# Kernel optimization log

Measured on AMD Instinct MI355X. Metric: run time of the kernel, lower is better.

## Reference

```python
import jax, jax.numpy as jnp
import numpy as np

DN = ('NCDHW', 'OIDHW', 'NCDHW')  # conv dimension numbers for 3D conv in torch layout
EPS = 1e-14


def setup_inputs() -> dict:
    key = jax.random.key(0)
    k1, k2 = jax.random.split(key)
    # xs: [B, C, D, H, W]
    xs = jax.random.normal(k1, (16, 128, 24, 24, 24), dtype=jnp.float32)
    # feature_vectors (prototypes): [num_features, C, w_1, h_1, L_1]
    feature_vectors = jax.random.normal(k2, (128, 128, 3, 3, 3), dtype=jnp.float32)
    return {"xs": xs, "feature_vectors": feature_vectors}


def reference(xs, feature_vectors):
    F_, C, kd, kh, kw = feature_vectors.shape
    # ||x_patch||^2: the original convolves xs**2 with all-ones weights of shape
    # [F, C, kd, kh, kw], producing F identical channels. We compute a single
    # sum-pool channel (same math) and let broadcasting supply the F channels.
    ones = jnp.ones((1, C, kd, kh, kw), dtype=xs.dtype)
    xs_squared_l2 = jax.lax.conv_general_dilated(
        xs * xs, ones, window_strides=(1, 1, 1), padding='VALID',
        dimension_numbers=DN)  # [B, 1, D', H', W']
    # ||p||^2 per prototype: [F, 1, 1, 1]
    ps_squared_l2 = jnp.sum(feature_vectors * feature_vectors,
                            axis=(1, 2, 3, 4)).reshape(-1, 1, 1, 1)
    # <x_patch, p>: the real weighted conv. [B, F, D', H', W']
    xs_conv = jax.lax.conv_general_dilated(
        xs, feature_vectors, window_strides=(1, 1, 1), padding='VALID',
        dimension_numbers=DN)
    distance = xs_squared_l2 + ps_squared_l2 - 2.0 * xs_conv
    return jnp.sqrt(jnp.abs(distance) + EPS)
```

## Files before the change

kernel.cpp:

```cpp
#include <hip/hip_runtime.h>
#include <hip/hip_bf16.h>

typedef __attribute__((ext_vector_type(8))) __bf16 bf16x8;
typedef __attribute__((ext_vector_type(2))) __bf16 bf16x2;
typedef __attribute__((ext_vector_type(4))) float f32x4;

#define B_   16
#define C_   128
#define DIM  24
#define F_   128
#define OD   22
#define OS   (OD*OD*OD)
#define SPB  (DIM*DIM*DIM)
#define K_   3456
#define M_   (B_*OS)
#define OUTN (B_*F_*OS)

__device__ __forceinline__ void async16(const void* g, void* l) {
  __builtin_amdgcn_global_load_lds(
      (const __attribute__((address_space(1))) unsigned int*)g,
      (__attribute__((address_space(3))) unsigned int*)l, 16, 0, 0);
}

__global__ __launch_bounds__(256) void prep_x(const float* __restrict__ xs,
                                              __bf16* __restrict__ xt,
                                              float* __restrict__ s1) {
  __shared__ float tile[C_ * 97];
  __shared__ float red[192];
  const int blk = blockIdx.x;
  const int yg = blk % 6;
  const int t2 = blk / 6;
  const int z = t2 % DIM;
  const int b = t2 / DIM;
  const int t = threadIdx.x;
  const float* src = xs + (size_t)b * C_ * SPB + z * (DIM * DIM) + yg * 96;
  for (int it = 0; it < 12; ++it) {
    int idx = it * 256 + t;
    int c = idx / 24, f4 = idx - c * 24;
    const float4 v = *(const float4*)(src + (size_t)c * SPB + f4 * 4);
    float* d = &tile[c * 97 + f4 * 4];
    d[0] = v.x; d[1] = v.y; d[2] = v.z; d[3] = v.w;
  }
  __syncthreads();
  size_t obase = ((size_t)b * SPB + z * (DIM * DIM) + yg * 96) * C_;
  for (int it = 0; it < 24; ++it) {
    int idx = it * 256 + t;
    int c2 = idx & 63, x = idx >> 6;
    bf16x2 v;
    v[0] = (__bf16)tile[(2 * c2) * 97 + x];
    v[1] = (__bf16)tile[(2 * c2 + 1) * 97 + x];
    *(bf16x2*)&xt[obase + (size_t)x * C_ + 2 * c2] = v;
  }
  if (t < 192) {
    int g = t / 96, p = t - g * 96;
    float s = 0.f;
    for (int c = g; c < C_; c += 2) {
      float v = tile[c * 97 + p];
      s += v * v;
    }
    red[g * 96 + p] = s;
  }
  __syncthreads();
  if (t < 96)
    s1[((size_t)b * SPB + z * (DIM * DIM) + yg * 96) + t] = red[t] + red[96 + t];
}

__global__ void prep_w(const float* __restrict__ fv, __bf16* __restrict__ Wt,
                       float* __restrict__ psq) {
  __shared__ float tile[K_];
  const int f = blockIdx.x;
  const float* src = fv + (size_t)f * K_;
  float part = 0.f;
  for (int idx = threadIdx.x; idx < K_; idx += 256) {
    float v = src[idx];
    tile[idx] = v;
    part += v * v;
  }
  __syncthreads();
  for (int idx = threadIdx.x; idx < K_; idx += 256) {
    int c = idx & 127, off = idx >> 7;
    Wt[(size_t)f * K_ + idx] = (__bf16)tile[c * 27 + off];
  }
  for (int o = 32; o > 0; o >>= 1) part += __shfl_down(part, o, 64);
  __shared__ float red[4];
  int w = threadIdx.x >> 6, l = threadIdx.x & 63;
  if (l == 0) red[w] = part;
  __syncthreads();
  if (threadIdx.x == 0) psq[f] = red[0] + red[1] + red[2] + red[3];
}

__global__ void pool_sq(const float* __restrict__ s1, float* __restrict__ xsq) {
  int i = blockIdx.x * 256 + threadIdx.x;
  if (i >= M_) return;
  int ow = i % OD;
  int t = i / OD;
  int oh = t % OD; t /= OD;
  int od = t % OD;
  int b = t / OD;
  const float* p = s1 + ((b * DIM + od) * DIM + oh) * DIM + ow;
  float s = 0.f;
#pragma unroll
  for (int dz = 0; dz < 3; ++dz)
#pragma unroll
    for (int dy = 0; dy < 3; ++dy)
#pragma unroll
      for (int dx = 0; dx < 3; ++dx)
        s += p[dz * 576 + dy * 24 + dx];
  xsq[i] = s;
}

__global__ __launch_bounds__(256, 2) void l2gemm(
    const __bf16* __restrict__ xt, const __bf16* __restrict__ Wt,
    const float* __restrict__ xsq, const float* __restrict__ psq,
    float* __restrict__ out) {
  __shared__ __align__(16) __bf16 Wl[128 * 64];
  __shared__ __align__(16) __bf16 Pl[256 * 64];
  const int t = threadIdx.x;
  const int l = t & 63, w = t >> 6;
  const int quad = l >> 4, lan = l & 15;
  const int e = t & 7, r0 = t >> 3;
  const int esw = (e ^ (r0 & 7)) * 8;

  const int nwg = gridDim.x;
  const int orig = blockIdx.x;
  const int xcd = orig & 7, lo = orig >> 3;
  const int q = nwg >> 3, r = nwg & 7;
  const int mt = (xcd < r ? xcd * (q + 1) : r * (q + 1) + (xcd - r) * q) + lo;

  int sb[8];
#pragma unroll
  for (int p = 0; p < 8; ++p) {
    int m = mt * 256 + r0 + 32 * p;
    if (m >= M_) m = M_ - 1;
    int b = m / OS;
    int s = m - b * OS;
    int od = s / (OD * OD);
    int s2 = s - od * (OD * OD);
    int oh = s2 / OD;
    int ow = s2 - oh * OD;
    sb[p] = b * SPB + od * 576 + oh * 24 + ow;
  }

  f32x4 acc[4][8];
#pragma unroll
  for (int i = 0; i < 4; ++i)
#pragma unroll
    for (int n = 0; n < 8; ++n) acc[i][n] = (f32x4){0.f, 0.f, 0.f, 0.f};

  const int wm = (w & 1) * 64;
  const int wn = (w >> 1) * 128;

#pragma unroll 1
  for (int kt = 0; kt < 54; ++kt) {
    {
      int off = kt >> 1;
      int dz = off / 9;
      int rem = off - dz * 9;
      int dy = rem / 3;
      int dx = rem - dy * 3;
      int doff = dz * 576 + dy * 24 + dx;
      int c0 = (kt & 1) << 6;
#pragma unroll
      for (int p = 0; p < 4; ++p) {
        const __bf16* gw = Wt + (size_t)(r0 + 32 * p) * K_ + kt * 64 + esw;
        async16(gw, &Wl[(size_t)(8 * w + 32 * p) * 64]);
      }
#pragma unroll
      for (int p = 0; p < 8; ++p) {
        const __bf16* gp = xt + (((size_t)(sb[p] + doff)) << 7) + c0 + esw;
        async16(gp, &Pl[(size_t)(8 * w + 32 * p) * 64]);
      }
    }
    __syncthreads();
#pragma unroll
    for (int kk = 0; kk < 2; ++kk) {
      const int swz = ((kk * 4 + quad) ^ (lan & 7)) * 8;
      bf16x8 a[4], bb[8];
#pragma unroll
      for (int i = 0; i < 4; ++i)
        a[i] = *(const bf16x8*)&Wl[(wm + i * 16 + lan) * 64 + swz];
#pragma unroll
      for (int n = 0; n < 8; ++n)
        bb[n] = *(const bf16x8*)&Pl[(wn + n * 16 + lan) * 64 + swz];
      __builtin_amdgcn_s_setprio(1);
#pragma unroll
      for (int i = 0; i < 4; ++i)
#pragma unroll
        for (int n = 0; n < 8; ++n)
          acc[i][n] = __builtin_amdgcn_mfma_f32_16x16x32_bf16(a[i], bb[n],
                                                              acc[i][n], 0, 0, 0);
      __builtin_amdgcn_s_setprio(0);
    }
    __syncthreads();
  }

  int mb[8], mok[8];
  float xv[8];
#pragma unroll
  for (int n = 0; n < 8; ++n) {
    int m = mt * 256 + wn + n * 16 + lan;
    mok[n] = (m < M_);
    if (m >= M_) m = M_ - 1;
    int b = m / OS;
    int s = m - b * OS;
    mb[n] = b * (F_ * OS) + s;
    xv[n] = xsq[m];
  }
#pragma unroll
  for (int i = 0; i < 4; ++i) {
#pragma unroll
    for (int r2 = 0; r2 < 4; ++r2) {
      int f = wm + i * 16 + quad * 4 + r2;
      float pq = psq[f];
#pragma unroll
      for (int n = 0; n < 8; ++n) {
        if (mok[n]) {
          float d = xv[n] + pq - 2.0f * acc[i][n][r2];
          out[mb[n] + f * OS] = sqrtf(fabsf(d) + 1e-14f);
        }
      }
    }
  }
}

__global__ void l2conv_direct(const float* __restrict__ xs,
                              const float* __restrict__ fv,
                              float* __restrict__ out) {
  int i = blockIdx.x * 256 + threadIdx.x;
  if (i >= OUTN) return;
  int s = i % OS;
  int t2 = i / OS;
  int f = t2 & 127;
  int b = t2 >> 7;
  int od = s / (OD * OD);
  int s2 = s - od * (OD * OD);
  int oh = s2 / OD;
  int ow = s2 - oh * OD;
  const float* xp = xs + (size_t)b * C_ * SPB + od * 576 + oh * 24 + ow;
  const float* wp = fv + (size_t)f * K_;
  float dot = 0.f, xq = 0.f, pq = 0.f;
  for (int c = 0; c < C_; ++c) {
    const float* xpc = xp + (size_t)c * SPB;
    const float* wpc = wp + c * 27;
#pragma unroll
    for (int o = 0; o < 27; ++o) {
      int dz = o / 9;
      int ry = o - dz * 9;
      int dy = ry / 3;
      int dx = ry - dy * 3;
      float xv = xpc[dz * 576 + dy * 24 + dx];
      float wv = wpc[o];
      dot += xv * wv;
      xq += xv * xv;
      pq += wv * wv;
    }
  }
  out[i] = sqrtf(fabsf(xq + pq - 2.f * dot) + 1e-14f);
}

extern "C" void kernel_launch(void* const* d_in, const int* in_sizes, int n_in,
                              void* d_out, int out_size, void* d_ws,
                              size_t ws_size, hipStream_t stream) {
  const float* xs = (const float*)d_in[0];
  const float* fv = (const float*)d_in[1];
  float* out = (float*)d_out;

  const size_t xt_b  = (size_t)B_ * SPB * C_ * 2;
  const size_t wt_b  = (size_t)F_ * K_ * 2;
  const size_t s1_b  = (size_t)B_ * SPB * 4;
  const size_t xsq_b = (size_t)M_ * 4;
  const size_t psq_b = 512;
  if (ws_size < xt_b + wt_b + s1_b + xsq_b + psq_b) {
    l2conv_direct<<<(OUTN + 255) / 256, 256, 0, stream>>>(xs, fv, out);
    return;
  }
  char* p = (char*)d_ws;
  __bf16* xt = (__bf16*)p;          p += xt_b;
  __bf16* Wt = (__bf16*)p;          p += wt_b;
  float*  s1 = (float*)p;           p += s1_b;
  float*  xsq = (float*)p;          p += xsq_b;
  float*  psq = (float*)p;

  prep_x<<<B_ * DIM * DIM / 4, 256, 0, stream>>>(xs, xt, s1);
  prep_w<<<F_, 256, 0, stream>>>(fv, Wt, psq);
  pool_sq<<<(M_ + 255) / 256, 256, 0, stream>>>(s1, xsq);
  l2gemm<<<(M_ + 255) / 256, 256, 0, stream>>>(xt, Wt, xsq, psq, out);
}
```

Before: 414.1 us.

## Switch implicit-GEMM conv to FP8 MFMA and fuse sum-pool into GEMM

Converts the activations and weights to FP8 e4m3 instead of bf16, with a permuted channel layout, and uses the 16x16x32 fp8 MFMA. This halves operand bytes and K-loop trips, so each tile loads all 128 channels per spatial offset. The pool_sq kernel is removed and the 3x3x3 sum of squares is computed inside the GEMM prologue into LDS. FP8 inputs cost considerable accuracy for a distance computed as a difference of large terms, so tolerance may be exceeded. Dropping the occupancy hint and doubling LDS also changes occupancy.

```diff
diff --git a/kernel.cpp b/kernel.cpp
--- a/kernel.cpp
+++ b/kernel.cpp
@@ -1,9 +1,9 @@
 #include <hip/hip_runtime.h>
 #include <hip/hip_bf16.h>
-
-typedef __attribute__((ext_vector_type(8))) __bf16 bf16x8;
-typedef __attribute__((ext_vector_type(2))) __bf16 bf16x2;
+#include <hip/hip_fp8.h>
+
 typedef __attribute__((ext_vector_type(4))) float f32x4;
+typedef __attribute__((ext_vector_type(2))) long i64x2;
 
 #define B_   16
 #define C_   128
@@ -22,8 +22,12 @@
       (__attribute__((address_space(3))) unsigned int*)l, 16, 0, 0);
 }
 
+__device__ __forceinline__ unsigned char f2fp8(float v) {
+  return __hip_fp8_e4m3(v).__x;
+}
+
 __global__ __launch_bounds__(256) void prep_x(const float* __restrict__ xs,
-                                              __bf16* __restrict__ xt,
+                                              unsigned char* __restrict__ xt,
                                               float* __restrict__ s1) {
   __shared__ float tile[C_ * 97];
   __shared__ float red[192];
@@ -43,13 +47,18 @@
   }
   __syncthreads();
   size_t obase = ((size_t)b * SPB + z * (DIM * DIM) + yg * 96) * C_;
-  for (int it = 0; it < 24; ++it) {
+  for (int it = 0; it < 6; ++it) {
     int idx = it * 256 + t;
-    int c2 = idx & 63, x = idx >> 6;
-    bf16x2 v;
-    v[0] = (__bf16)tile[(2 * c2) * 97 + x];
-    v[1] = (__bf16)tile[(2 * c2 + 1) * 97 + x];
-    *(bf16x2*)&xt[obase + (size_t)x * C_ + 2 * c2] = v;
+    int s = idx & 15, x = idx >> 4;
+    int g = (s & 3) * 4 + (s >> 2);
+    unsigned int w0 = 0, w1 = 0;
+#pragma unroll
+    for (int j = 0; j < 4; ++j)
+      w0 |= ((unsigned int)f2fp8(tile[(8 * g + j) * 97 + x])) << (8 * j);
+#pragma unroll
+    for (int j = 0; j < 4; ++j)
+      w1 |= ((unsigned int)f2fp8(tile[(8 * g + 4 + j) * 97 + x])) << (8 * j);
+    *(uint2*)&xt[obase + (size_t)x * C_ + s * 8] = make_uint2(w0, w1);
   }
   if (t < 192) {
     int g = t / 96, p = t - g * 96;
@@ -65,7 +74,8 @@
     s1[((size_t)b * SPB + z * (DIM * DIM) + yg * 96) + t] = red[t] + red[96 + t];
 }
 
-__global__ void prep_w(const float* __restrict__ fv, __bf16* __restrict__ Wt,
+__global__ void prep_w(const float* __restrict__ fv,
+                       unsigned char* __restrict__ Wt,
                        float* __restrict__ psq) {
   __shared__ float tile[K_];
   const int f = blockIdx.x;
@@ -79,7 +89,8 @@
   __syncthreads();
   for (int idx = threadIdx.x; idx < K_; idx += 256) {
     int c = idx & 127, off = idx >> 7;
-    Wt[(size_t)f * K_ + idx] = (__bf16)tile[c * 27 + off];
+    int pos = off * 128 + ((c >> 3) & 3) * 32 + (c >> 5) * 8 + (c & 7);
+    Wt[(size_t)f * K_ + pos] = f2fp8(tile[c * 27 + off]);
   }
   for (int o = 32; o > 0; o >>= 1) part += __shfl_down(part, o, 64);
   __shared__ float red[4];
@@ -89,37 +100,18 @@
   if (threadIdx.x == 0) psq[f] = red[0] + red[1] + red[2] + red[3];
 }
 
-__global__ void pool_sq(const float* __restrict__ s1, float* __restrict__ xsq) {
-  int i = blockIdx.x * 256 + threadIdx.x;
-  if (i >= M_) return;
-  int ow = i % OD;
-  int t = i / OD;
-  int oh = t % OD; t /= OD;
-  int od = t % OD;
-  int b = t / OD;
-  const float* p = s1 + ((b * DIM + od) * DIM + oh) * DIM + ow;
-  float s = 0.f;
-#pragma unroll
-  for (int dz = 0; dz < 3; ++dz)
-#pragma unroll
-    for (int dy = 0; dy < 3; ++dy)
-#pragma unroll
-      for (int dx = 0; dx < 3; ++dx)
-        s += p[dz * 576 + dy * 24 + dx];
-  xsq[i] = s;
-}
-
-__global__ __launch_bounds__(256, 2) void l2gemm(
-    const __bf16* __restrict__ xt, const __bf16* __restrict__ Wt,
-    const float* __restrict__ xsq, const float* __restrict__ psq,
+__global__ __launch_bounds__(256) void l2gemm(
+    const unsigned char* __restrict__ xt, const unsigned char* __restrict__ Wt,
+    const float* __restrict__ s1, const float* __restrict__ psq,
     float* __restrict__ out) {
-  __shared__ __align__(16) __bf16 Wl[128 * 64];
-  __shared__ __align__(16) __bf16 Pl[256 * 64];
+  __shared__ __align__(16) unsigned char Wl[128 * 128];
+  __shared__ __align__(16) unsigned char Pl[256 * 128];
+  __shared__ float xsql[256];
   const int t = threadIdx.x;
   const int l = t & 63, w = t >> 6;
   const int quad = l >> 4, lan = l & 15;
   const int e = t & 7, r0 = t >> 3;
-  const int esw = (e ^ (r0 & 7)) * 8;
+  const int esw = (e ^ (r0 & 7)) * 16;
 
   const int nwg = gridDim.x;
   const int orig = blockIdx.x;
@@ -141,6 +133,27 @@
     sb[p] = b * SPB + od * 576 + oh * 24 + ow;
   }
 
+  {
+    int m = mt * 256 + t;
+    if (m >= M_) m = M_ - 1;
+    int b = m / OS;
+    int s = m - b * OS;
+    int od = s / (OD * OD);
+    int s2 = s - od * (OD * OD);
+    int oh = s2 / OD;
+    int ow = s2 - oh * OD;
+    const float* pp = s1 + ((b * DIM + od) * DIM + oh) * DIM + ow;
+    float ss = 0.f;
+#pragma unroll
+    for (int dz = 0; dz < 3; ++dz)
+#pragma unroll
+      for (int dy = 0; dy < 3; ++dy)
+#pragma unroll
+        for (int dx = 0; dx < 3; ++dx)
+          ss += pp[dz * 576 + dy * 24 + dx];
+    xsql[t] = ss;
+  }
+
   f32x4 acc[4][8];
 #pragma unroll
   for (int i = 0; i < 4; ++i)
@@ -151,44 +164,44 @@
   const int wn = (w >> 1) * 128;
 
 #pragma unroll 1
-  for (int kt = 0; kt < 54; ++kt) {
+  for (int kt = 0; kt < 27; ++kt) {
     {
-      int off = kt >> 1;
-      int dz = off / 9;
-      int rem = off - dz * 9;
+      int dz = kt / 9;
+      int rem = kt - dz * 9;
       int dy = rem / 3;
       int dx = rem - dy * 3;
       int doff = dz * 576 + dy * 24 + dx;
-      int c0 = (kt & 1) << 6;
 #pragma unroll
       for (int p = 0; p < 4; ++p) {
-        const __bf16* gw = Wt + (size_t)(r0 + 32 * p) * K_ + kt * 64 + esw;
-        async16(gw, &Wl[(size_t)(8 * w + 32 * p) * 64]);
+        const unsigned char* gw = Wt + (size_t)(r0 + 32 * p) * K_ + kt * 128 + esw;
+        async16(gw, &Wl[(size_t)(8 * w + 32 * p) * 128]);
       }
 #pragma unroll
       for (int p = 0; p < 8; ++p) {
-        const __bf16* gp = xt + (((size_t)(sb[p] + doff)) << 7) + c0 + esw;
-        async16(gp, &Pl[(size_t)(8 * w + 32 * p) * 64]);
+        const unsigned char* gp = xt + (size_t)(sb[p] + doff) * 128 + esw;
+        async16(gp, &Pl[(size_t)(8 * w + 32 * p) * 128]);
       }
     }
     __syncthreads();
 #pragma unroll
-    for (int kk = 0; kk < 2; ++kk) {
-      const int swz = ((kk * 4 + quad) ^ (lan & 7)) * 8;
-      bf16x8 a[4], bb[8];
+    for (int kkp = 0; kkp < 2; ++kkp) {
+      const int swz = (((quad << 1) | kkp) ^ (lan & 7)) * 16;
+      i64x2 a2[4], b2[8];
 #pragma unroll
       for (int i = 0; i < 4; ++i)
-        a[i] = *(const bf16x8*)&Wl[(wm + i * 16 + lan) * 64 + swz];
+        a2[i] = *(const i64x2*)&Wl[(wm + i * 16 + lan) * 128 + swz];
 #pragma unroll
       for (int n = 0; n < 8; ++n)
-        bb[n] = *(const bf16x8*)&Pl[(wn + n * 16 + lan) * 64 + swz];
+        b2[n] = *(const i64x2*)&Pl[(wn + n * 16 + lan) * 128 + swz];
       __builtin_amdgcn_s_setprio(1);
 #pragma unroll
-      for (int i = 0; i < 4; ++i)
-#pragma unroll
-        for (int n = 0; n < 8; ++n)
-          acc[i][n] = __builtin_amdgcn_mfma_f32_16x16x32_bf16(a[i], bb[n],
-                                                              acc[i][n], 0, 0, 0);
+      for (int h = 0; h < 2; ++h)
+#pragma unroll
+        for (int i = 0; i < 4; ++i)
+#pragma unroll
+          for (int n = 0; n < 8; ++n)
+            acc[i][n] = __builtin_amdgcn_mfma_f32_16x16x32_fp8_fp8(
+                a2[i][h], b2[n][h], acc[i][n], 0, 0, 0);
       __builtin_amdgcn_s_setprio(0);
     }
     __syncthreads();
@@ -204,7 +217,7 @@
     int b = m / OS;
     int s = m - b * OS;
     mb[n] = b * (F_ * OS) + s;
-    xv[n] = xsq[m];
+    xv[n] = xsql[wn + n * 16 + lan];
   }
 #pragma unroll
   for (int i = 0; i < 4; ++i) {
@@ -265,24 +278,21 @@
   const float* fv = (const float*)d_in[1];
   float* out = (float*)d_out;
 
-  const size_t xt_b  = (size_t)B_ * SPB * C_ * 2;
-  const size_t wt_b  = (size_t)F_ * K_ * 2;
+  const size_t xt_b  = (size_t)B_ * SPB * C_;
+  const size_t wt_b  = (size_t)F_ * K_;
   const size_t s1_b  = (size_t)B_ * SPB * 4;
-  const size_t xsq_b = (size_t)M_ * 4;
   const size_t psq_b = 512;
-  if (ws_size < xt_b + wt_b + s1_b + xsq_b + psq_b) {
+  if (ws_size < xt_b + wt_b + s1_b + psq_b) {
     l2conv_direct<<<(OUTN + 255) / 256, 256, 0, stream>>>(xs, fv, out);
     return;
   }
   char* p = (char*)d_ws;
-  __bf16* xt = (__bf16*)p;          p += xt_b;
-  __bf16* Wt = (__bf16*)p;          p += wt_b;
-  float*  s1 = (float*)p;           p += s1_b;
-  float*  xsq = (float*)p;          p += xsq_b;
-  float*  psq = (float*)p;
+  unsigned char* xt = (unsigned char*)p;  p += xt_b;
+  unsigned char* Wt = (unsigned char*)p;  p += wt_b;
+  float* s1 = (float*)p;                  p += s1_b;
+  float* psq = (float*)p;
 
   prep_x<<<B_ * DIM * DIM / 4, 256, 0, stream>>>(xs, xt, s1);
   prep_w<<<F_, 256, 0, stream>>>(fv, Wt, psq);
-  pool_sq<<<(M_ + 255) / 256, 256, 0, stream>>>(s1, xsq);
-  l2gemm<<<(M_ + 255) / 256, 256, 0, stream>>>(xt, Wt, xsq, psq, out);
-}
+  l2gemm<<<(M_ + 255) / 256, 256, 0, stream>>>(xt, Wt, s1, psq, out);
+}
```

Measured after the change: 451.6 us. 1.09x slower.
